# Optimization experiments

Hardware: AMD Instinct MI355X
Metric: run time of the kernel (lower is better)

## Reference

```python
import jax, jax.numpy as jnp
import numpy as np

N_OUTER, M_INNER = 32, 128      # triples shape (n, m, 3)
N = N_OUTER * M_INNER            # 4096 entity pairs
L = 256                          # max_relation_pairs (padded neighbour list length)
K = 256                          # relation embedding dim
R = 50000                        # number of relations / predicates
NEG_INF = -1e30


def setup_inputs() -> dict:
    key = jax.random.key(0)
    k1, k2, k3, k4, k5, k6 = jax.random.split(key, 6)
    table = jax.random.normal(k1, (R, K), dtype=jnp.float32) * 0.02
    w1 = jax.random.normal(k2, (N, L), dtype=jnp.float32)
    w2 = jax.random.normal(k3, (N, L), dtype=jnp.float32)
    cand_idx = jax.random.randint(k4, (N,), 0, R, dtype=jnp.int32)
    neigh_idx = jax.random.randint(k5, (N, L), 0, R, dtype=jnp.int32)
    # ragged lengths in [1, L] (each entity pair has at least one neighbour)
    lengths = jax.random.randint(k6, (N,), 1, L + 1, dtype=jnp.int32)
    return {"table": table, "w1": w1, "w2": w2,
            "cand_idx": cand_idx, "neigh_idx": neigh_idx, "lengths": lengths}


def reference(table, w1, w2, cand_idx, neigh_idx, lengths):
    # mask out padded neighbour slots
    mask = jnp.arange(L, dtype=jnp.int32)[None, :] < lengths[:, None]  # [N, L]
    cand = table[cand_idx]          # [N, K] candidate relation embeds
    neigh = table[neigh_idx]        # [N, L, K] ragged neighbour embeds (padded)
    # dual_attention_logit_aggregator: lw = w1 + w2; normalize by logsumexp; exp -> weights
    lw = jnp.where(mask, w1 + w2, NEG_INF)                        # [N, L]
    lw = lw - jax.nn.logsumexp(lw, axis=1, keepdims=True)         # stable log-softmax
    weights = jnp.exp(lw)                                         # padding -> 0
    agg = jnp.einsum('nl,nlk->nk', weights, neigh)                # weighted sum [N, K]
    # forward score: (weighted_sums * candidate_relation_embeds).sum(-1).view(n, m)
    return (agg * cand).sum(axis=-1).reshape(N_OUTER, M_INNER)
```

## Files before the change

kernel.cpp:

```cpp
#include <hip/hip_runtime.h>
#include <hip/hip_fp16.h>
#include <math.h>

#define NROWS 4096
#define LMAX  256
#define KDIM  256
#define NREL  50000
#define NCELL 8
#define RPC   6250
#define NBN   16
#define NNB   (NROWS / NBN)
#define NQ    (NNB * NCELL)
#define QCAP  512

#define TH_BYTES  ((size_t)NREL * KDIM * 2)
#define Q_BYTES   ((size_t)NQ * QCAP * 8)
#define QC_BYTES  ((size_t)NQ * 4)
#define WS_NEEDED (TH_BYTES + Q_BYTES + QC_BYTES)

typedef float    f32x4  __attribute__((ext_vector_type(4)));
typedef unsigned u32x4  __attribute__((ext_vector_type(4)));
typedef _Float16 h16x2  __attribute__((ext_vector_type(2)));

__device__ __forceinline__ h16x2 as_h2(unsigned u) {
    union { unsigned u; h16x2 h; } x; x.u = u; return x.h;
}

#if __has_builtin(__builtin_amdgcn_fdot2)
__device__ __forceinline__ float dot4h(uint2 a, uint2 b) {
    float d = __builtin_amdgcn_fdot2(as_h2(a.x), as_h2(b.x), 0.0f, false);
    return  __builtin_amdgcn_fdot2(as_h2(a.y), as_h2(b.y), d,    false);
}
#else
__device__ __forceinline__ float dot4h(uint2 a, uint2 b) {
    const __half2* pa = (const __half2*)&a;
    const __half2* pb = (const __half2*)&b;
    const float2 a0 = __half22float2(pa[0]), b0 = __half22float2(pb[0]);
    const float2 a1 = __half22float2(pa[1]), b1 = __half22float2(pb[1]);
    float d = a0.x * b0.x;
    d = fmaf(a0.y, b0.y, d);
    d = fmaf(a1.x, b1.x, d);
    return fmaf(a1.y, b1.y, d);
}
#endif

__device__ __forceinline__ unsigned cell_of(unsigned idx) {
    return (idx * 21475u) >> 27;
}

__global__ __launch_bounds__(256) void convert_kernel(
    const float* __restrict__ table, __half* __restrict__ tH,
    unsigned* __restrict__ qcount)
{
    const int tid = threadIdx.x;
    if (blockIdx.x == 0) {
        #pragma unroll
        for (int i = 0; i < NQ / 256; ++i)
            qcount[tid + 256 * i] = 0u;
    }
    const int cell = blockIdx.x & 7;
    const int rg   = blockIdx.x >> 3;
    const int rloc = rg * 4 + (tid >> 6);
    if (rloc >= RPC) return;
    const int r    = cell * RPC + rloc;
    const int lane = tid & 63;

    const f32x4 f = __builtin_nontemporal_load(
        (const f32x4*)(table + (size_t)r * KDIM + lane * 4));
    __half2 hh[2];
    hh[0] = __floats2half2_rn(f.x, f.y);
    hh[1] = __floats2half2_rn(f.z, f.w);
    *(uint2*)(tH + (size_t)r * KDIM + lane * 4) = *(const uint2*)hh;
}

__global__ __launch_bounds__(256) void pass1_softmax(
    const float* __restrict__ w1,
    const float* __restrict__ w2,
    const int*   __restrict__ neigh_idx,
    const int*   __restrict__ lengths,
    uint2*       __restrict__ queues,
    unsigned*    __restrict__ qcount,
    float*       __restrict__ out)
{
    const int n   = blockIdx.x;
    const int tid = threadIdx.x;

    __shared__ float    s_red[4];
    __shared__ float    s_b;
    __shared__ unsigned l_cnt[8], l_base[8];

    const int len = lengths[n];
    if (tid < 8) l_cnt[tid] = 0u;

    float v = -INFINITY;
    if (tid < len) {
        const float a = __builtin_nontemporal_load(&w1[(size_t)n * LMAX + tid]);
        const float b = __builtin_nontemporal_load(&w2[(size_t)n * LMAX + tid]);
        v = a + b;
    }
    const unsigned idx =
        (unsigned)__builtin_nontemporal_load(&neigh_idx[(size_t)n * LMAX + tid]);

    float m = v;
    #pragma unroll
    for (int off = 32; off >= 1; off >>= 1)
        m = fmaxf(m, __shfl_down(m, off, 64));
    if ((tid & 63) == 0) s_red[tid >> 6] = m;
    __syncthreads();
    if (tid == 0)
        s_b = fmaxf(fmaxf(s_red[0], s_red[1]), fmaxf(s_red[2], s_red[3]));
    __syncthreads();
    m = s_b;

    const float e = (tid < len) ? __expf(v - m) : 0.0f;
    float s = e;
    #pragma unroll
    for (int off = 32; off >= 1; off >>= 1)
        s += __shfl_down(s, off, 64);
    if ((tid & 63) == 0) s_red[tid >> 6] = s;
    __syncthreads();
    if (tid == 0) s_b = s_red[0] + s_red[1] + s_red[2] + s_red[3];
    __syncthreads();

    const float w = e * (1.0f / s_b);

    unsigned cell = 0, rank = 0;
    if (tid < len) {
        cell = cell_of(idx);
        rank = atomicAdd(&l_cnt[cell], 1u);
    }
    __syncthreads();
    if (tid < 8)
        l_base[tid] = atomicAdd(&qcount[(unsigned)(n >> 4) * 8u + tid],
                                l_cnt[tid]);
    __syncthreads();
    if (tid < len) {
        const unsigned pos = l_base[cell] + rank;
        if (pos < QCAP) {
            const unsigned lrow = idx - cell * RPC;
            queues[(size_t)((unsigned)(n >> 4) * 8u + cell) * QCAP + pos] =
                make_uint2((lrow << 6) | (unsigned)(n & 15),
                           __float_as_uint(w));
        }
    }

    if (tid == 0) out[n] = 0.0f;
}

#define CONSUME(rr, tt, pp) do {                                             \
    const unsigned nl_ = (rr).x & 63u;                                       \
    if (nl_ != cur) {                         \
        float red_ = accd;                                                   \
        red_ += __shfl_down(red_, 32, 64); red_ += __shfl_down(red_, 16, 64);\
        red_ += __shfl_down(red_,  8, 64); red_ += __shfl_down(red_,  4, 64);\
        red_ += __shfl_down(red_,  2, 64); red_ += __shfl_down(red_,  1, 64);\
        if (lane == 0) atomicAdd(&s_acc[cur], red_);                         \
        accd = 0.0f; cur = nl_;                                              \
    }                                                                        \
    if ((pp) < end) {                           \
        const float w_ = __uint_as_float((rr).y);                            \
        const uint2 cc_ = *(const uint2*)&s_cand[nl_][lane * 4];             \
        accd = fmaf(w_, dot4h((tt), cc_), accd);                             \
    }                                                                        \
} while (0)

__global__ __launch_bounds__(256) void gather_kernel(
    const __half*   __restrict__ tH,
    const int*      __restrict__ cand_idx,
    const uint2*    __restrict__ queues,
    const unsigned* __restrict__ qcount,
    float*          __restrict__ out)
{
    const int qid  = blockIdx.x;
    const int cell = qid & 7;
    const int nb   = qid >> 3;
    const int tid  = threadIdx.x;
    const int lane = tid & 63;
    const int wv   = tid >> 6;

    __shared__ __align__(16) __half s_cand[NBN][KDIM];
    __shared__ __align__(16) uint2  s_q[QCAP];
    __shared__ float s_acc[NBN];

    const unsigned count = min(qcount[qid], (unsigned)QCAP);
    if (tid < NBN) s_acc[tid] = 0.0f;

    for (int c = tid; c < NBN * 64; c += 256) {
        const int i = c >> 6, off = c & 63;
        const int ci = cand_idx[nb * NBN + i];
        *(uint2*)&s_cand[i][off * 4] =
            *(const uint2*)&tH[(size_t)ci * KDIM + off * 4];
    }
    const u32x4* qg = (const u32x4*)(queues + (size_t)qid * QCAP);
    for (int i = tid; 2 * i < (int)count; i += 256) {
        const u32x4 qv = __builtin_nontemporal_load(qg + i);
        *((u32x4*)s_q + i) = qv;
    }
    __syncthreads();

    if (count) {
        const __half* sl = tH + (size_t)cell * RPC * KDIM;
        const unsigned per   = (count + 3) >> 2;
        const unsigned start = wv * per;
        const unsigned end   = min(start + per, count);
        if (start < end) {
            const unsigned e1 = end - 1;
            unsigned cur = s_q[start].x & 63u;
            float accd = 0.0f;
            for (unsigned b = start; b < end; b += 4) {
                const unsigned p1 = min(b + 1, e1);
                const unsigned p2 = min(b + 2, e1);
                const unsigned p3 = min(b + 3, e1);
                const uint2 r0 = s_q[b],  r1 = s_q[p1];
                const uint2 r2 = s_q[p2], r3 = s_q[p3];
                const uint2 t0 = *(const uint2*)&sl[(size_t)(r0.x >> 6) * KDIM + lane * 4];
                const uint2 t1 = *(const uint2*)&sl[(size_t)(r1.x >> 6) * KDIM + lane * 4];
                const uint2 t2 = *(const uint2*)&sl[(size_t)(r2.x >> 6) * KDIM + lane * 4];
                const uint2 t3 = *(const uint2*)&sl[(size_t)(r3.x >> 6) * KDIM + lane * 4];
                __builtin_amdgcn_sched_barrier(0);
                CONSUME(r0, t0, b);
                CONSUME(r1, t1, b + 1);
                CONSUME(r2, t2, b + 2);
                CONSUME(r3, t3, b + 3);
            }
            float red = accd;
            red += __shfl_down(red, 32, 64); red += __shfl_down(red, 16, 64);
            red += __shfl_down(red,  8, 64); red += __shfl_down(red,  4, 64);
            red += __shfl_down(red,  2, 64); red += __shfl_down(red,  1, 64);
            if (lane == 0) atomicAdd(&s_acc[cur], red);
        }
    }
    __syncthreads();
    if (tid < NBN) atomicAdd(&out[nb * NBN + tid], s_acc[tid]);
}

__global__ __launch_bounds__(256) void epanre_fallback(
    const float* __restrict__ table,
    const float* __restrict__ w1,
    const float* __restrict__ w2,
    const int*   __restrict__ cand_idx,
    const int*   __restrict__ neigh_idx,
    const int*   __restrict__ lengths,
    float*       __restrict__ out)
{
    const int n   = blockIdx.x;
    const int tid = threadIdx.x;

    __shared__ __align__(16) float s_w[LMAX];
    __shared__ int   s_idx[LMAX];
    __shared__ __align__(16) float s_cand[KDIM];
    __shared__ float s_red[4];
    __shared__ float s_bcast;

    const int len = lengths[n];

    float v = -INFINITY;
    if (tid < len) v = w1[(size_t)n * LMAX + tid] + w2[(size_t)n * LMAX + tid];
    s_idx[tid]  = neigh_idx[(size_t)n * LMAX + tid];
    s_cand[tid] = table[(size_t)cand_idx[n] * KDIM + tid];

    float m = v;
    #pragma unroll
    for (int off = 32; off >= 1; off >>= 1)
        m = fmaxf(m, __shfl_down(m, off, 64));
    if ((tid & 63) == 0) s_red[tid >> 6] = m;
    __syncthreads();
    if (tid == 0)
        s_bcast = fmaxf(fmaxf(s_red[0], s_red[1]), fmaxf(s_red[2], s_red[3]));
    __syncthreads();
    m = s_bcast;

    float e = (tid < len) ? __expf(v - m) : 0.0f;
    float s = e;
    #pragma unroll
    for (int off = 32; off >= 1; off >>= 1)
        s += __shfl_down(s, off, 64);
    if ((tid & 63) == 0) s_red[tid >> 6] = s;
    __syncthreads();
    if (tid == 0) s_bcast = s_red[0] + s_red[1] + s_red[2] + s_red[3];
    __syncthreads();
    const float inv = 1.0f / s_bcast;
    s_w[tid] = e * inv;
    __syncthreads();

    const int g    = tid >> 6;
    const int lane = tid & 63;
    const float4* tab4 = (const float4*)table;
    float4 acc = make_float4(0.f, 0.f, 0.f, 0.f);

    for (int l0 = 0; l0 < len; l0 += 4) {
        const int   l = l0 + g;
        const float w = (l < len) ? s_w[l] : 0.0f;
        const int   idx = s_idx[l];
        const float4 t = tab4[(size_t)idx * (KDIM / 4) + lane];
        acc.x = fmaf(w, t.x, acc.x);
        acc.y = fmaf(w, t.y, acc.y);
        acc.z = fmaf(w, t.z, acc.z);
        acc.w = fmaf(w, t.w, acc.w);
    }

    const float4 c = ((const float4*)s_cand)[lane];
    float partial = acc.x * c.x + acc.y * c.y + acc.z * c.z + acc.w * c.w;
    #pragma unroll
    for (int off = 32; off >= 1; off >>= 1)
        partial += __shfl_down(partial, off, 64);
    if (lane == 0) s_red[g] = partial;
    __syncthreads();
    if (tid == 0) out[n] = s_red[0] + s_red[1] + s_red[2] + s_red[3];
}

extern "C" void kernel_launch(void* const* d_in, const int* in_sizes, int n_in,
                              void* d_out, int out_size, void* d_ws, size_t ws_size,
                              hipStream_t stream) {
    const float* table     = (const float*)d_in[0];
    const float* w1        = (const float*)d_in[1];
    const float* w2        = (const float*)d_in[2];
    const int*   cand_idx  = (const int*)d_in[3];
    const int*   neigh_idx = (const int*)d_in[4];
    const int*   lengths   = (const int*)d_in[5];
    float* out = (float*)d_out;

    if (ws_size < WS_NEEDED) {
        epanre_fallback<<<NROWS, 256, 0, stream>>>(table, w1, w2, cand_idx,
                                                   neigh_idx, lengths, out);
        return;
    }

    __half*   tH     = (__half*)d_ws;
    uint2*    queues = (uint2*)((char*)d_ws + TH_BYTES);
    unsigned* qcount = (unsigned*)((char*)d_ws + TH_BYTES + Q_BYTES);

    const int rgs = (RPC + 3) / 4;
    convert_kernel<<<rgs * NCELL, 256, 0, stream>>>(table, tH, qcount);
    pass1_softmax<<<NROWS, 256, 0, stream>>>(w1, w2, neigh_idx, lengths,
                                             queues, qcount, out);
    gather_kernel<<<NQ, 256, 0, stream>>>(tH, cand_idx, queues, qcount, out);
}
```

Measured before the change: 53.07 us.

## Fuse table conversion and softmax prep into one kernel, one wave per row

Merges the fp32-to-fp16 table conversion and the per-row softmax/queue-binning pass into a single launch, with block ranges assigned to each role. The softmax part now handles one row per wavefront with vectorized 4-wide loads and xor-shuffle reductions, removing block-wide barriers and shrinking the grid for that phase. Zeroing of the queue counters moves to a hipMemsetAsync, so the launch count stays the same, but the two independent phases can now overlap. It relies on intra-wave ordering of LDS atomics without explicit barriers.

```diff
diff --git a/kernel.cpp b/kernel.cpp
--- a/kernel.cpp
+++ b/kernel.cpp
@@ -12,6 +12,7 @@
 #define NNB   (NROWS / NBN)
 #define NQ    (NNB * NCELL)
 #define QCAP  512
+#define SMB   (NROWS / 4)
 
 #define TH_BYTES  ((size_t)NREL * KDIM * 2)
 #define Q_BYTES   ((size_t)NQ * QCAP * 8)
@@ -48,103 +49,97 @@
     return (idx * 21475u) >> 27;
 }
 
-__global__ __launch_bounds__(256) void convert_kernel(
-    const float* __restrict__ table, __half* __restrict__ tH,
-    unsigned* __restrict__ qcount)
-{
-    const int tid = threadIdx.x;
-    if (blockIdx.x == 0) {
-        #pragma unroll
-        for (int i = 0; i < NQ / 256; ++i)
-            qcount[tid + 256 * i] = 0u;
-    }
-    const int cell = blockIdx.x & 7;
-    const int rg   = blockIdx.x >> 3;
-    const int rloc = rg * 4 + (tid >> 6);
-    if (rloc >= RPC) return;
-    const int r    = cell * RPC + rloc;
-    const int lane = tid & 63;
-
-    const f32x4 f = __builtin_nontemporal_load(
-        (const f32x4*)(table + (size_t)r * KDIM + lane * 4));
-    __half2 hh[2];
-    hh[0] = __floats2half2_rn(f.x, f.y);
-    hh[1] = __floats2half2_rn(f.z, f.w);
-    *(uint2*)(tH + (size_t)r * KDIM + lane * 4) = *(const uint2*)hh;
-}
-
-__global__ __launch_bounds__(256) void pass1_softmax(
+__global__ __launch_bounds__(256) void fused_prep(
+    const float* __restrict__ table,
     const float* __restrict__ w1,
     const float* __restrict__ w2,
     const int*   __restrict__ neigh_idx,
     const int*   __restrict__ lengths,
+    __half*      __restrict__ tH,
     uint2*       __restrict__ queues,
     unsigned*    __restrict__ qcount,
     float*       __restrict__ out)
 {
-    const int n   = blockIdx.x;
-    const int tid = threadIdx.x;
-
-    __shared__ float    s_red[4];
-    __shared__ float    s_b;
-    __shared__ unsigned l_cnt[8], l_base[8];
-
-    const int len = lengths[n];
-    if (tid < 8) l_cnt[tid] = 0u;
-
-    float v = -INFINITY;
-    if (tid < len) {
-        const float a = __builtin_nontemporal_load(&w1[(size_t)n * LMAX + tid]);
-        const float b = __builtin_nontemporal_load(&w2[(size_t)n * LMAX + tid]);
-        v = a + b;
-    }
-    const unsigned idx =
-        (unsigned)__builtin_nontemporal_load(&neigh_idx[(size_t)n * LMAX + tid]);
-
-    float m = v;
-    #pragma unroll
-    for (int off = 32; off >= 1; off >>= 1)
-        m = fmaxf(m, __shfl_down(m, off, 64));
-    if ((tid & 63) == 0) s_red[tid >> 6] = m;
-    __syncthreads();
-    if (tid == 0)
-        s_b = fmaxf(fmaxf(s_red[0], s_red[1]), fmaxf(s_red[2], s_red[3]));
-    __syncthreads();
-    m = s_b;
-
-    const float e = (tid < len) ? __expf(v - m) : 0.0f;
-    float s = e;
-    #pragma unroll
-    for (int off = 32; off >= 1; off >>= 1)
-        s += __shfl_down(s, off, 64);
-    if ((tid & 63) == 0) s_red[tid >> 6] = s;
-    __syncthreads();
-    if (tid == 0) s_b = s_red[0] + s_red[1] + s_red[2] + s_red[3];
-    __syncthreads();
-
-    const float w = e * (1.0f / s_b);
-
-    unsigned cell = 0, rank = 0;
-    if (tid < len) {
-        cell = cell_of(idx);
-        rank = atomicAdd(&l_cnt[cell], 1u);
-    }
-    __syncthreads();
-    if (tid < 8)
-        l_base[tid] = atomicAdd(&qcount[(unsigned)(n >> 4) * 8u + tid],
-                                l_cnt[tid]);
-    __syncthreads();
-    if (tid < len) {
-        const unsigned pos = l_base[cell] + rank;
-        if (pos < QCAP) {
-            const unsigned lrow = idx - cell * RPC;
-            queues[(size_t)((unsigned)(n >> 4) * 8u + cell) * QCAP + pos] =
-                make_uint2((lrow << 6) | (unsigned)(n & 15),
-                           __float_as_uint(w));
+    const int tid  = threadIdx.x;
+    const int lane = tid & 63;
+    const int wv   = tid >> 6;
+
+    if (blockIdx.x < SMB) {
+        const int n   = blockIdx.x * 4 + wv;
+        const int len = lengths[n];
+
+        __shared__ unsigned l_cnt[4][8], l_base[4][8];
+
+        const f32x4 a = __builtin_nontemporal_load(
+            (const f32x4*)(w1 + (size_t)n * LMAX) + lane);
+        const f32x4 b = __builtin_nontemporal_load(
+            (const f32x4*)(w2 + (size_t)n * LMAX) + lane);
+        const u32x4 ii = __builtin_nontemporal_load(
+            (const u32x4*)(neigh_idx + (size_t)n * LMAX) + lane);
+
+        float v[4];
+        #pragma unroll
+        for (int j = 0; j < 4; ++j)
+            v[j] = (lane * 4 + j < len) ? (a[j] + b[j]) : -INFINITY;
+
+        float m = fmaxf(fmaxf(v[0], v[1]), fmaxf(v[2], v[3]));
+        #pragma unroll
+        for (int off = 32; off >= 1; off >>= 1)
+            m = fmaxf(m, __shfl_xor(m, off, 64));
+
+        float e[4];
+        float s = 0.0f;
+        #pragma unroll
+        for (int j = 0; j < 4; ++j) {
+            e[j] = (lane * 4 + j < len) ? __expf(v[j] - m) : 0.0f;
+            s += e[j];
         }
-    }
-
-    if (tid == 0) out[n] = 0.0f;
+        #pragma unroll
+        for (int off = 32; off >= 1; off >>= 1)
+            s += __shfl_xor(s, off, 64);
+        const float inv = 1.0f / s;
+
+        if (lane < 8) l_cnt[wv][lane] = 0u;
+
+        unsigned cc[4] = {0, 0, 0, 0}, rk[4] = {0, 0, 0, 0};
+        #pragma unroll
+        for (int j = 0; j < 4; ++j) {
+            if (lane * 4 + j < len) {
+                cc[j] = cell_of(ii[j]);
+                rk[j] = atomicAdd(&l_cnt[wv][cc[j]], 1u);
+            }
+        }
+        if (lane < 8)
+            l_base[wv][lane] = atomicAdd(&qcount[(unsigned)(n >> 4) * 8u + lane],
+                                         l_cnt[wv][lane]);
+        #pragma unroll
+        for (int j = 0; j < 4; ++j) {
+            if (lane * 4 + j < len) {
+                const unsigned pos = l_base[wv][cc[j]] + rk[j];
+                if (pos < QCAP) {
+                    const unsigned lrow = ii[j] - cc[j] * RPC;
+                    queues[(size_t)((unsigned)(n >> 4) * 8u + cc[j]) * QCAP + pos] =
+                        make_uint2((lrow << 6) | (unsigned)(n & 15),
+                                   __float_as_uint(e[j] * inv));
+                }
+            }
+        }
+        if (lane == 0) out[n] = 0.0f;
+    } else {
+        const int bb   = blockIdx.x - SMB;
+        const int cell = bb & 7;
+        const int rg   = bb >> 3;
+        const int rloc = rg * 4 + wv;
+        if (rloc >= RPC) return;
+        const int r = cell * RPC + rloc;
+
+        const f32x4 f = __builtin_nontemporal_load(
+            (const f32x4*)(table + (size_t)r * KDIM + lane * 4));
+        __half2 hh[2];
+        hh[0] = __floats2half2_rn(f.x, f.y);
+        hh[1] = __floats2half2_rn(f.z, f.w);
+        *(uint2*)(tH + (size_t)r * KDIM + lane * 4) = *(const uint2*)hh;
+    }
 }
 
 #define CONSUME(rr, tt, pp) do {                                             \
@@ -330,9 +325,11 @@
     uint2*    queues = (uint2*)((char*)d_ws + TH_BYTES);
     unsigned* qcount = (unsigned*)((char*)d_ws + TH_BYTES + Q_BYTES);
 
+    hipMemsetAsync(qcount, 0, QC_BYTES, stream);
+
     const int rgs = (RPC + 3) / 4;
-    convert_kernel<<<rgs * NCELL, 256, 0, stream>>>(table, tH, qcount);
-    pass1_softmax<<<NROWS, 256, 0, stream>>>(w1, w2, neigh_idx, lengths,
-                                             queues, qcount, out);
+    fused_prep<<<SMB + rgs * NCELL, 256, 0, stream>>>(table, w1, w2,
+                                                      neigh_idx, lengths,
+                                                      tH, queues, qcount, out);
     gather_kernel<<<NQ, 256, 0, stream>>>(tH, cand_idx, queues, qcount, out);
 }
```

Measured after the change: 52.69 us. No clear change (-0.7%).
